# Kernel optimization log

Measured on AMD Instinct MI355X. Metric: run time of the kernel, lower is better.

The kernel has to match this reference:

```python
import jax, jax.numpy as jnp
import numpy as np

B, S, D, H = 4, 2048, 1024, 16
DK = D // H


def setup_inputs() -> dict:
    key = jax.random.key(0)
    ks = jax.random.split(key, 11)
    std = 1.0 / np.sqrt(D)
    mk = lambda k: jax.random.uniform(k, (D, D), jnp.float32, -std, std)
    mb = lambda k: jax.random.uniform(k, (D,), jnp.float32, -std, std)
    return {
        "query": jax.random.normal(ks[0], (B, S, D), jnp.float32),
        "key": jax.random.normal(ks[1], (B, S, D), jnp.float32),
        "value": jax.random.normal(ks[2], (B, S, D), jnp.float32),
        "Wq": mk(ks[3]), "bq": mb(ks[4]),
        "Wk": mk(ks[5]), "bk": mb(ks[6]),
        "Wv": mk(ks[7]), "bv": mb(ks[8]),
        "Wo": mk(ks[9]), "bo": mb(ks[10]),
    }


def reference(query, key, value, Wq, bq, Wk, bk, Wv, bv, Wo, bo):
    # Linear projections (torch Linear: x @ W.T + b)
    Q = query @ Wq.T + bq   # [B,S,D]
    K = key @ Wk.T + bk
    V = value @ Wv.T + bv
    # split heads -> [B,H,S,DK]
    Q = Q.reshape(B, S, H, DK).transpose(0, 2, 1, 3)
    K = K.reshape(B, S, H, DK).transpose(0, 2, 1, 3)
    V = V.reshape(B, S, H, DK).transpose(0, 2, 1, 3)
    scale = 1.0 / jnp.sqrt(jnp.asarray(DK, Q.dtype))
    scores = jnp.einsum("bhqd,bhkd->bhqk", Q, K) * scale  # [B,H,S,S]
    attn = jax.nn.softmax(scores, axis=-1)
    out = jnp.einsum("bhqk,bhkd->bhqd", attn, V)          # [B,H,S,DK]
    out = out.transpose(0, 2, 1, 3).reshape(B, S, D)       # [B,S,D]
    return out @ Wo.T + bo
```

## Files before the change

### kernel.cpp

```cpp
#include <hip/hip_runtime.h>
#include <hip/hip_bf16.h>
#include <stdint.h>


using f32x4  = __attribute__((ext_vector_type(4))) float;
using f32x16 = __attribute__((ext_vector_type(16))) float;
using s16x8  = __attribute__((ext_vector_type(8))) short;
using u16x8  = __attribute__((ext_vector_type(8))) unsigned short;
using u16x4  = __attribute__((ext_vector_type(4))) unsigned short;

#define MFMA16(a, b, c) __builtin_amdgcn_mfma_f32_16x16x32_bf16((a), (b), (c), 0, 0, 0)
#define MFMA32(a, b, c) __builtin_amdgcn_mfma_f32_32x32x16_bf16((a), (b), (c), 0, 0, 0)

#define GLL16(gptr, lptr)                                                      \
  __builtin_amdgcn_global_load_lds(                                            \
      (const __attribute__((address_space(1))) void*)(gptr),                   \
      (__attribute__((address_space(3))) void*)(lptr), 16, 0, 0)

__device__ __forceinline__ unsigned short f2bf(float f) {
  union { __hip_bfloat16 h; unsigned short u; } cv;
  cv.h = __float2bfloat16(f);
  return cv.u;
}

__device__ __forceinline__ unsigned int pkrne(float a, float b) {
  unsigned int ua = __builtin_bit_cast(unsigned int, a);
  unsigned int ub = __builtin_bit_cast(unsigned int, b);
  ua = ua + 0x7FFFu + ((ua >> 16) & 1u);
  ub = ub + 0x7FFFu + ((ub >> 16) & 1u);
  return (ua >> 16) | (ub & 0xFFFF0000u);
}

__device__ __forceinline__ float exp2a(float x) {
  return __builtin_amdgcn_exp2f(x);
}

__global__ __launch_bounds__(256) void cast_w_kernel(
    const float* __restrict__ wq, const float* __restrict__ wk,
    const float* __restrict__ wv, const float* __restrict__ wo,
    unsigned short* __restrict__ dst) {
  int i = blockIdx.x * 256 + threadIdx.x;
  int m = i >> 18;
  int off = i & 0x3FFFF;
  const float* src = (m == 0) ? wq : (m == 1) ? wk : (m == 2) ? wv : wo;
  float4 v = reinterpret_cast<const float4*>(src)[off];
  u16x4 o;
  o[0] = f2bf(v.x); o[1] = f2bf(v.y); o[2] = f2bf(v.z); o[3] = f2bf(v.w);
  *reinterpret_cast<u16x4*>(dst + (size_t)i * 4) = o;
}

__global__ __launch_bounds__(256) void cast_x_kernel(
    const float* __restrict__ src, unsigned short* __restrict__ dst) {
  int i = blockIdx.x * 256 + threadIdx.x;
  float4 v = reinterpret_cast<const float4*>(src)[i];
  uint2 p;
  p.x = pkrne(v.x, v.y);
  p.y = pkrne(v.z, v.w);
  *reinterpret_cast<uint2*>(dst + (size_t)i * 4) = p;
}

__global__ __launch_bounds__(256) void gemm_qkvz_kernel(
    const unsigned short* __restrict__ Xbf, const unsigned short* __restrict__ W,
    const float* __restrict__ bias, unsigned short* __restrict__ dst,
    float qscale) {
  __shared__ __align__(16) unsigned short Asm_[128 * 64];
  __shared__ __align__(16) unsigned short Bsm_[128 * 64];

  const int t = threadIdx.x;
  const int lane = t & 63, w = t >> 6;
  const int g = lane >> 4, c = lane & 15;
  const int wm = (w >> 1) * 64, wn = (w & 1) * 64;
  const int n0 = (blockIdx.y & 7) * 128;
  const int m0 = (blockIdx.x * 8 + (blockIdx.y >> 3)) * 128;

  f32x4 acc[4][4];
#pragma unroll
  for (int i = 0; i < 4; i++)
#pragma unroll
    for (int j = 0; j < 4; j++) acc[i][j] = (f32x4)0.0f;

  const int blr = lane >> 3;
  const int bgc = (lane & 7) ^ blr;

  for (int kt = 0; kt < 16; ++kt) {
    const int k0 = kt * 64;
    __syncthreads();
#pragma unroll
    for (int i = 0; i < 4; i++) {
      int ii = w * 4 + i;
      const unsigned short* ga = Xbf + (size_t)(m0 + ii * 8 + blr) * 1024 + k0 + bgc * 8;
      GLL16(ga, &Asm_[ii * 512]);
      const unsigned short* gb = W + (size_t)(n0 + ii * 8 + blr) * 1024 + k0 + bgc * 8;
      GLL16(gb, &Bsm_[ii * 512]);
    }
    __syncthreads();

#pragma unroll
    for (int ks = 0; ks < 2; ks++) {
      s16x8 af[4], bfr[4];
#pragma unroll
      for (int mt = 0; mt < 4; mt++) {
        int r = wm + mt * 16 + c;
        af[mt] = *reinterpret_cast<const s16x8*>(&Asm_[r * 64 + (((ks * 4 + g) ^ (c & 7)) << 3)]);
      }
#pragma unroll
      for (int nt = 0; nt < 4; nt++) {
        int r = wn + nt * 16 + c;
        bfr[nt] = *reinterpret_cast<const s16x8*>(&Bsm_[r * 64 + (((ks * 4 + g) ^ (c & 7)) << 3)]);
      }
#pragma unroll
      for (int mt = 0; mt < 4; mt++)
#pragma unroll
        for (int nt = 0; nt < 4; nt++)
          acc[mt][nt] = MFMA16(af[mt], bfr[nt], acc[mt][nt]);
    }
  }

#pragma unroll
  for (int mt = 0; mt < 4; mt++)
#pragma unroll
    for (int nt = 0; nt < 4; nt++) {
      int n = n0 + wn + nt * 16 + c;
      float bb = bias[n];
      int h = n >> 6, dk = n & 63;
#pragma unroll
      for (int r = 0; r < 4; r++) {
        int m = m0 + wm + mt * 16 + g * 4 + r;
        int b = m >> 11, s = m & 2047;
        dst[(((size_t)b * 16 + h) * 2048 + s) * 64 + dk] =
            f2bf((acc[mt][nt][r] + bb) * qscale);
      }
    }
}

__global__ __launch_bounds__(256) void gemm_out_kernel(
    const unsigned short* __restrict__ AO, const unsigned short* __restrict__ Wo,
    const float* __restrict__ bo, float* __restrict__ out) {
  __shared__ __align__(16) unsigned short Asm_[128 * 64];
  __shared__ __align__(16) unsigned short Bsm_[128 * 64];

  const int t = threadIdx.x;
  const int lane = t & 63, w = t >> 6;
  const int g = lane >> 4, c = lane & 15;
  const int wm = (w >> 1) * 64, wn = (w & 1) * 64;
  const int n0 = (blockIdx.y & 7) * 128;
  const int m0 = (blockIdx.x * 8 + (blockIdx.y >> 3)) * 128;

  f32x4 acc[4][4];
#pragma unroll
  for (int i = 0; i < 4; i++)
#pragma unroll
    for (int j = 0; j < 4; j++) acc[i][j] = (f32x4)0.0f;

  const int blr = lane >> 3;
  const int bgc = (lane & 7) ^ blr;

  for (int kt = 0; kt < 16; ++kt) {
    const int k0 = kt * 64;
    __syncthreads();
#pragma unroll
    for (int i = 0; i < 4; i++) {
      int ii = w * 4 + i;
      const unsigned short* ga = AO + (size_t)(m0 + ii * 8 + blr) * 1024 + k0 + bgc * 8;
      GLL16(ga, &Asm_[ii * 512]);
      const unsigned short* gb = Wo + (size_t)(n0 + ii * 8 + blr) * 1024 + k0 + bgc * 8;
      GLL16(gb, &Bsm_[ii * 512]);
    }
    __syncthreads();

#pragma unroll
    for (int ks = 0; ks < 2; ks++) {
      s16x8 af[4], bfr[4];
#pragma unroll
      for (int mt = 0; mt < 4; mt++) {
        int r = wm + mt * 16 + c;
        af[mt] = *reinterpret_cast<const s16x8*>(&Asm_[r * 64 + (((ks * 4 + g) ^ (c & 7)) << 3)]);
      }
#pragma unroll
      for (int nt = 0; nt < 4; nt++) {
        int r = wn + nt * 16 + c;
        bfr[nt] = *reinterpret_cast<const s16x8*>(&Bsm_[r * 64 + (((ks * 4 + g) ^ (c & 7)) << 3)]);
      }
#pragma unroll
      for (int mt = 0; mt < 4; mt++)
#pragma unroll
        for (int nt = 0; nt < 4; nt++)
          acc[mt][nt] = MFMA16(af[mt], bfr[nt], acc[mt][nt]);
    }
  }

#pragma unroll
  for (int mt = 0; mt < 4; mt++)
#pragma unroll
    for (int nt = 0; nt < 4; nt++) {
      int n = n0 + wn + nt * 16 + c;
      float bb = bo[n];
#pragma unroll
      for (int r = 0; r < 4; r++) {
        int m = m0 + wm + mt * 16 + g * 4 + r;
        out[(size_t)m * 1024 + n] = acc[mt][nt][r] + bb;
      }
    }
}

__global__ __launch_bounds__(512) void attn_kernel(
    const unsigned short* __restrict__ Qh, const unsigned short* __restrict__ Kh,
    const unsigned short* __restrict__ Vh, unsigned short* __restrict__ AO) {
  const int bh = blockIdx.x * 8 + (blockIdx.y >> 3);
  const int b = bh >> 4, h = bh & 15;
  const int q0 = (blockIdx.y & 7) * 256;
  const int t = threadIdx.x, lane = t & 63, w = t >> 6;
  const int lo = lane & 31, hi = lane >> 5;

  __shared__ __align__(16) unsigned short Ks[2][64 * 64];
  __shared__ __align__(16) unsigned short Vt[2][64 * 64];

  const size_t kvbase = (size_t)bh * 2048 * 64;

  s16x8 qb[4];
  {
    const unsigned short* qp = Qh + kvbase + (size_t)(q0 + w * 32 + lo) * 64;
#pragma unroll
    for (int ks = 0; ks < 4; ks++)
      qb[ks] = *reinterpret_cast<const s16x8*>(qp + ks * 16 + hi * 8);
  }

  f32x16 oacc[2];
  oacc[0] = (f32x16)0.0f; oacc[1] = (f32x16)0.0f;
  float lsum = 0.0f;

  const int skrow = t >> 3, sks = t & 7;
  const int kgc = sks ^ (skrow & 7) ^ w;
  const int vkrow = t >> 3, vd0 = (t & 7) * 8;
  const int vwc = w ^ (t & 7);
  const int vcl = vkrow & 7;

  const int rx0 = (lo & 7) ^ (lo >> 3);
  const int rx1 = (lo & 7) ^ (4 | (lo >> 3));

  uint4 kk, vv;
  kk = *reinterpret_cast<const uint4*>(Kh + kvbase + (size_t)skrow * 64 + kgc * 8);
  vv = *reinterpret_cast<const uint4*>(Vh + kvbase + (size_t)vkrow * 64 + vd0);
  *reinterpret_cast<uint4*>(&Ks[0][(size_t)t * 8]) = kk;
  {
    const unsigned short* vs = reinterpret_cast<const unsigned short*>(&vv);
#pragma unroll
    for (int j = 0; j < 8; j++)
      Vt[0][(vd0 + j) * 64 + ((vwc ^ j) << 3) + vcl] = vs[j];
  }

  for (int it = 0; it < 32; ++it) {
    const int cur = it & 1, nxt = cur ^ 1;
    const bool more = (it < 31);
    if (more) {
      const int kv = (it + 1) * 64;
      kk = *reinterpret_cast<const uint4*>(Kh + kvbase + (size_t)(kv + skrow) * 64 + kgc * 8);
      vv = *reinterpret_cast<const uint4*>(Vh + kvbase + (size_t)(kv + vkrow) * 64 + vd0);
    }
    __syncthreads();

    f32x16 st[2];
    st[0] = (f32x16)0.0f; st[1] = (f32x16)0.0f;
#pragma unroll
    for (int kb = 0; kb < 2; kb++) {
      const int rx = kb ? rx1 : rx0;
#pragma unroll
      for (int ks = 0; ks < 4; ks++) {
        s16x8 ka = *reinterpret_cast<const s16x8*>(
            &Ks[cur][(kb * 32 + lo) * 64 + (((ks * 2 + hi) ^ rx) << 3)]);
        st[kb] = MFMA32(ka, qb[ks], st[kb]);
      }
    }

    s16x8 pa[4];
    float s0 = 0.0f, s1 = 0.0f, s2 = 0.0f, s3 = 0.0f;
#pragma unroll
    for (int kb = 0; kb < 2; kb++) {
      float e[16];
#pragma unroll
      for (int r = 0; r < 16; r += 4) {
        e[r]     = exp2a(st[kb][r]);
        e[r + 1] = exp2a(st[kb][r + 1]);
        e[r + 2] = exp2a(st[kb][r + 2]);
        e[r + 3] = exp2a(st[kb][r + 3]);
        s0 += e[r]; s1 += e[r + 1]; s2 += e[r + 2]; s3 += e[r + 3];
      }
#pragma unroll
      for (int half = 0; half < 2; half++) {
        const float* eb = e + half * 8;
        unsigned int x1 = pkrne(eb[0], eb[1]);
        unsigned int x2 = pkrne(eb[2], eb[3]);
        unsigned int y1 = pkrne(eb[4], eb[5]);
        unsigned int y2 = pkrne(eb[6], eb[7]);
        asm volatile("v_permlane32_swap_b32 %0, %1" : "+v"(x1), "+v"(y1));
        asm volatile("v_permlane32_swap_b32 %0, %1" : "+v"(x2), "+v"(y2));
        uint4 u;
        u.x = x1; u.y = x2; u.z = y1; u.w = y2;
        pa[kb * 2 + half] = *reinterpret_cast<const s16x8*>(&u);
      }
    }
    lsum += (s0 + s1) + (s2 + s3);

    if (more) {
      *reinterpret_cast<uint4*>(&Ks[nxt][(size_t)t * 8]) = kk;
      const unsigned short* vs = reinterpret_cast<const unsigned short*>(&vv);
#pragma unroll
      for (int j = 0; j < 8; j++)
        Vt[nxt][(vd0 + j) * 64 + ((vwc ^ j) << 3) + vcl] = vs[j];
    }

#pragma unroll
    for (int ks = 0; ks < 4; ks++)
#pragma unroll
      for (int db = 0; db < 2; db++) {
        const int rx = db ? rx1 : rx0;
        s16x8 vb = *reinterpret_cast<const s16x8*>(
            &Vt[cur][(db * 32 + lo) * 64 + (((ks * 2 + hi) ^ rx) << 3)]);
        oacc[db] = MFMA32(pa[ks], vb, oacc[db]);
      }
  }

  float ltot = lsum + __shfl_xor(lsum, 32);
  float linv = 1.0f / ltot;
#pragma unroll
  for (int r = 0; r < 16; r++) {
    int qr = (r & 3) + ((r >> 2) << 3) + (hi << 2);
    float inv_r = __shfl(linv, qr);
    int srow = q0 + w * 32 + qr;
    size_t obase = ((size_t)b * 2048 + srow) * 1024 + (size_t)h * 64;
    AO[obase + lo]      = f2bf(oacc[0][r] * inv_r);
    AO[obase + 32 + lo] = f2bf(oacc[1][r] * inv_r);
  }
}

extern "C" void kernel_launch(void* const* d_in, const int* in_sizes, int n_in,
                              void* d_out, int out_size, void* d_ws, size_t ws_size,
                              hipStream_t stream) {
  const float* query = (const float*)d_in[0];
  const float* key   = (const float*)d_in[1];
  const float* value = (const float*)d_in[2];
  const float* Wq = (const float*)d_in[3];
  const float* bq = (const float*)d_in[4];
  const float* Wk = (const float*)d_in[5];
  const float* bk = (const float*)d_in[6];
  const float* Wv = (const float*)d_in[7];
  const float* bv = (const float*)d_in[8];
  const float* Wo = (const float*)d_in[9];
  const float* bo = (const float*)d_in[10];

  uint8_t* wsb = (uint8_t*)d_ws;
  unsigned short* wbf = (unsigned short*)wsb;
  unsigned short* Qh  = (unsigned short*)(wsb + 8388608);
  unsigned short* Kh  = (unsigned short*)(wsb + 8388608 + 16777216);
  unsigned short* Vh  = (unsigned short*)(wsb + 8388608 + 2 * 16777216);
  unsigned short* AO  = (unsigned short*)(wsb + 8388608 + 3 * 16777216);
  unsigned short* Xbf = AO;

  const float QSCALE = 0.18033688011112042f;

  cast_w_kernel<<<dim3(4096), dim3(256), 0, stream>>>(Wq, Wk, Wv, Wo, wbf);

  cast_x_kernel<<<dim3(8192), dim3(256), 0, stream>>>(query, Xbf);
  gemm_qkvz_kernel<<<dim3(8, 64), dim3(256), 0, stream>>>(
      Xbf, wbf + (size_t)0 * 1048576, bq, Qh, QSCALE);
  cast_x_kernel<<<dim3(8192), dim3(256), 0, stream>>>(key, Xbf);
  gemm_qkvz_kernel<<<dim3(8, 64), dim3(256), 0, stream>>>(
      Xbf, wbf + (size_t)1 * 1048576, bk, Kh, 1.0f);
  cast_x_kernel<<<dim3(8192), dim3(256), 0, stream>>>(value, Xbf);
  gemm_qkvz_kernel<<<dim3(8, 64), dim3(256), 0, stream>>>(
      Xbf, wbf + (size_t)2 * 1048576, bv, Vh, 1.0f);

  attn_kernel<<<dim3(8, 64), dim3(512), 0, stream>>>(Qh, Kh, Vh, AO);
  gemm_out_kernel<<<dim3(8, 64), dim3(256), 0, stream>>>(
      AO, wbf + (size_t)3 * 1048576, bo, (float*)d_out);
}
```

Baseline: 229.5 us.

## Batch QKV casts and GEMMs into single launches; compute softmax row sums via MFMA

Combines the three input casts into one 3D-grid launch and the three projection GEMMs into one launch indexed by blockIdx.z, staging the key/value bf16 copies in the output buffer so all three can coexist. This cuts launch count and lets the three GEMMs fill the GPU together instead of running as separate under-filled waves. In the attention kernel, the per-row softmax denominator is now accumulated by an extra MFMA against a ones vector instead of scalar adds plus cross-lane shuffles. That adds four MFMAs per tile and a 16-register accumulator, and sums bf16-rounded probabilities, which matches the numerator's rounding.

```diff
diff --git a/kernel.cpp b/kernel.cpp
--- a/kernel.cpp
+++ b/kernel.cpp
@@ -49,20 +49,34 @@
   *reinterpret_cast<u16x4*>(dst + (size_t)i * 4) = o;
 }
 
-__global__ __launch_bounds__(256) void cast_x_kernel(
-    const float* __restrict__ src, unsigned short* __restrict__ dst) {
+__global__ __launch_bounds__(256) void cast_x3_kernel(
+    const float* __restrict__ q, const float* __restrict__ k,
+    const float* __restrict__ v, unsigned short* __restrict__ xq,
+    unsigned short* __restrict__ xk, unsigned short* __restrict__ xv) {
+  const int z = blockIdx.y;
+  const float* src = (z == 0) ? q : (z == 1) ? k : v;
+  unsigned short* dst = (z == 0) ? xq : (z == 1) ? xk : xv;
   int i = blockIdx.x * 256 + threadIdx.x;
-  float4 v = reinterpret_cast<const float4*>(src)[i];
+  float4 f = reinterpret_cast<const float4*>(src)[i];
   uint2 p;
-  p.x = pkrne(v.x, v.y);
-  p.y = pkrne(v.z, v.w);
+  p.x = pkrne(f.x, f.y);
+  p.y = pkrne(f.z, f.w);
   *reinterpret_cast<uint2*>(dst + (size_t)i * 4) = p;
 }
 
-__global__ __launch_bounds__(256) void gemm_qkvz_kernel(
-    const unsigned short* __restrict__ Xbf, const unsigned short* __restrict__ W,
-    const float* __restrict__ bias, unsigned short* __restrict__ dst,
-    float qscale) {
+__global__ __launch_bounds__(256) void gemm_qkv_kernel(
+    const unsigned short* __restrict__ Xq, const unsigned short* __restrict__ Xk,
+    const unsigned short* __restrict__ Xv, const unsigned short* __restrict__ wbf,
+    const float* __restrict__ bq, const float* __restrict__ bk,
+    const float* __restrict__ bv, unsigned short* __restrict__ Qh,
+    unsigned short* __restrict__ Kh, unsigned short* __restrict__ Vh) {
+  const int z = blockIdx.z;
+  const unsigned short* Xbf = (z == 0) ? Xq : (z == 1) ? Xk : Xv;
+  const unsigned short* W = wbf + (size_t)z * 1048576;
+  const float* bias = (z == 0) ? bq : (z == 1) ? bk : bv;
+  unsigned short* dst = (z == 0) ? Qh : (z == 1) ? Kh : Vh;
+  const float qscale = (z == 0) ? 0.18033688011112042f : 1.0f;
+
   __shared__ __align__(16) unsigned short Asm_[128 * 64];
   __shared__ __align__(16) unsigned short Bsm_[128 * 64];
 
@@ -225,9 +239,15 @@
       qb[ks] = *reinterpret_cast<const s16x8*>(qp + ks * 16 + hi * 8);
   }
 
-  f32x16 oacc[2];
-  oacc[0] = (f32x16)0.0f; oacc[1] = (f32x16)0.0f;
-  float lsum = 0.0f;
+  s16x8 onesb;
+  {
+    uint4 u;
+    u.x = 0x3F803F80u; u.y = 0x3F803F80u; u.z = 0x3F803F80u; u.w = 0x3F803F80u;
+    onesb = *reinterpret_cast<const s16x8*>(&u);
+  }
+
+  f32x16 oacc[2], lacc;
+  oacc[0] = (f32x16)0.0f; oacc[1] = (f32x16)0.0f; lacc = (f32x16)0.0f;
 
   const int skrow = t >> 3, sks = t & 7;
   const int kgc = sks ^ (skrow & 7) ^ w;
@@ -273,18 +293,11 @@
     }
 
     s16x8 pa[4];
-    float s0 = 0.0f, s1 = 0.0f, s2 = 0.0f, s3 = 0.0f;
 #pragma unroll
     for (int kb = 0; kb < 2; kb++) {
       float e[16];
 #pragma unroll
-      for (int r = 0; r < 16; r += 4) {
-        e[r]     = exp2a(st[kb][r]);
-        e[r + 1] = exp2a(st[kb][r + 1]);
-        e[r + 2] = exp2a(st[kb][r + 2]);
-        e[r + 3] = exp2a(st[kb][r + 3]);
-        s0 += e[r]; s1 += e[r + 1]; s2 += e[r + 2]; s3 += e[r + 3];
-      }
+      for (int r = 0; r < 16; r++) e[r] = exp2a(st[kb][r]);
 #pragma unroll
       for (int half = 0; half < 2; half++) {
         const float* eb = e + half * 8;
@@ -299,7 +312,9 @@
         pa[kb * 2 + half] = *reinterpret_cast<const s16x8*>(&u);
       }
     }
-    lsum += (s0 + s1) + (s2 + s3);
+
+#pragma unroll
+    for (int ks = 0; ks < 4; ks++) lacc = MFMA32(pa[ks], onesb, lacc);
 
     if (more) {
       *reinterpret_cast<uint4*>(&Ks[nxt][(size_t)t * 8]) = kk;
@@ -320,12 +335,10 @@
       }
   }
 
-  float ltot = lsum + __shfl_xor(lsum, 32);
-  float linv = 1.0f / ltot;
 #pragma unroll
   for (int r = 0; r < 16; r++) {
+    float inv_r = 1.0f / lacc[r];
     int qr = (r & 3) + ((r >> 2) << 3) + (hi << 2);
-    float inv_r = __shfl(linv, qr);
     int srow = q0 + w * 32 + qr;
     size_t obase = ((size_t)b * 2048 + srow) * 1024 + (size_t)h * 64;
     AO[obase + lo]      = f2bf(oacc[0][r] * inv_r);
@@ -354,22 +367,15 @@
   unsigned short* Kh  = (unsigned short*)(wsb + 8388608 + 16777216);
   unsigned short* Vh  = (unsigned short*)(wsb + 8388608 + 2 * 16777216);
   unsigned short* AO  = (unsigned short*)(wsb + 8388608 + 3 * 16777216);
-  unsigned short* Xbf = AO;
-
-  const float QSCALE = 0.18033688011112042f;
+  unsigned short* Xq = AO;
+  unsigned short* Xk = (unsigned short*)d_out;
+  unsigned short* Xv = (unsigned short*)d_out + 8388608;
 
   cast_w_kernel<<<dim3(4096), dim3(256), 0, stream>>>(Wq, Wk, Wv, Wo, wbf);
-
-  cast_x_kernel<<<dim3(8192), dim3(256), 0, stream>>>(query, Xbf);
-  gemm_qkvz_kernel<<<dim3(8, 64), dim3(256), 0, stream>>>(
-      Xbf, wbf + (size_t)0 * 1048576, bq, Qh, QSCALE);
-  cast_x_kernel<<<dim3(8192), dim3(256), 0, stream>>>(key, Xbf);
-  gemm_qkvz_kernel<<<dim3(8, 64), dim3(256), 0, stream>>>(
-      Xbf, wbf + (size_t)1 * 1048576, bk, Kh, 1.0f);
-  cast_x_kernel<<<dim3(8192), dim3(256), 0, stream>>>(value, Xbf);
-  gemm_qkvz_kernel<<<dim3(8, 64), dim3(256), 0, stream>>>(
-      Xbf, wbf + (size_t)2 * 1048576, bv, Vh, 1.0f);
-
+  cast_x3_kernel<<<dim3(8192, 3), dim3(256), 0, stream>>>(
+      query, key, value, Xq, Xk, Xv);
+  gemm_qkv_kernel<<<dim3(8, 64, 3), dim3(256), 0, stream>>>(
+      Xq, Xk, Xv, wbf, bq, bk, bv, Qh, Kh, Vh);
   attn_kernel<<<dim3(8, 64), dim3(512), 0, stream>>>(Qh, Kh, Vh, AO);
   gemm_out_kernel<<<dim3(8, 64), dim3(256), 0, stream>>>(
       AO, wbf + (size_t)3 * 1048576, bo, (float*)d_out);
```

After: 217.4 us. 5.3% less time.
